# Performance work log

Measured on AMD Instinct MI355X. Metric: run time of the kernel, lower is better.

## Reference

```python
import jax, jax.numpy as jnp
import numpy as np


def _level_layout(depth, arity):
    counts = [arity ** (depth - 1 - l) for l in range(depth)]  # leaves first
    offs = np.concatenate([[0], np.cumsum(counts)]).astype(np.int64)
    return counts, offs


def _tree_lstm_forward(x, e2h_w, ioux_w, ioux_b, iouh_w, iouh_b,
                       fx_w, fx_b, fh_w, fh_b,
                       children_idx, edge_type, depth, arity):
    N = x.shape[0]
    H = fh_w.shape[0]
    E = e2h_w.shape[0]
    counts, offs = _level_layout(depth, arity)

    # state tables; row N is the zero-state sentinel for padded/leaf children
    h_all = jnp.zeros((N + 1, H), x.dtype)
    c_all = jnp.zeros((N + 1, H), x.dtype)

    # --- leaves (level 0): child_h_sum = 0, sum(f*child_c) = 0 ---
    nL = counts[0]
    iou = x[:nL] @ ioux_w.T + ioux_b + iouh_b  # iouh(0) = bias
    i, o, u = jnp.split(iou, 3, axis=1)
    c = jax.nn.sigmoid(i) * jnp.tanh(u)
    h = jax.nn.sigmoid(o) * jnp.tanh(c)
    c_all = c_all.at[:nL].set(c)
    h_all = h_all.at[:nL].set(h)

    # --- internal levels, bottom-up ---
    for l in range(1, depth):
        s, e = int(offs[l]), int(offs[l + 1])
        idx = children_idx[s:e]          # [M, C]
        et = edge_type[s:e]              # [M, C]
        ch_h = h_all[idx]                # [M, C, H]
        ch_c = c_all[idx]                # [M, C, H]
        xm = x[s:e]                      # [M, D]
        # edge-typed aggregation: sum_k W_{e_k} h_k = sum_e W_e (sum_{k: e_k=e} h_k)
        onehot = jax.nn.one_hot(et, E, dtype=x.dtype)       # [M, C, E]
        S = jnp.einsum('mce,mcj->mej', onehot, ch_h)        # [M, E, H]
        hsum = jnp.einsum('mej,eij->mi', S, e2h_w)          # [M, H]
        iou = xm @ ioux_w.T + ioux_b + hsum @ iouh_w.T + iouh_b
        i, o, u = jnp.split(iou, 3, axis=1)
        f = jax.nn.sigmoid(jnp.einsum('mcj,ij->mci', ch_h, fh_w) + fh_b
                           + (xm @ fx_w.T + fx_b)[:, None, :])  # [M, C, H]
        fc = (f * ch_c).sum(axis=1)                             # [M, H]
        c = jax.nn.sigmoid(i) * jnp.tanh(u) + fc
        h = jax.nn.sigmoid(o) * jnp.tanh(c)
        c_all = c_all.at[s:e].set(c)
        h_all = h_all.at[s:e].set(h)

    root = N - 1
    return c_all[root:root + 1], h_all[root:root + 1]


def setup_inputs() -> dict:
    key = jax.random.key(0)
    ks = jax.random.split(key, 12)
    depth, arity, E, H, D = 9, 4, 37, 256, 300
    counts, offs = _level_layout(depth, arity)
    N = int(offs[-1])  # 87381

    # complete arity-ary tree, reverse level order (leaves first, root last)
    children = np.full((N, arity), N, dtype=np.int32)  # sentinel N for leaves
    for l in range(1, depth):
        p = np.arange(counts[l])
        base = offs[l - 1] + p * arity
        children[offs[l]:offs[l + 1]] = (base[:, None] + np.arange(arity)[None, :]).astype(np.int32)

    sc = 0.05
    return {
        'x': jax.random.normal(ks[0], (N, D), jnp.float32),
        'children_idx': jnp.asarray(children),
        'edge_type': jax.random.randint(ks[1], (N, arity), 0, E, jnp.int32),
        'depth': depth,
        'arity': arity,
        'e2h_w': jax.random.normal(ks[2], (E, H, H), jnp.float32) * sc,
        'ioux_w': jax.random.normal(ks[3], (3 * H, D), jnp.float32) * sc,
        'ioux_b': jax.random.normal(ks[4], (3 * H,), jnp.float32) * sc,
        'iouh_w': jax.random.normal(ks[5], (3 * H, H), jnp.float32) * sc,
        'iouh_b': jax.random.normal(ks[6], (3 * H,), jnp.float32) * sc,
        'fx_w': jax.random.normal(ks[7], (H, D), jnp.float32) * sc,
        'fx_b': jax.random.normal(ks[8], (H,), jnp.float32) * sc,
        'fh_w': jax.random.normal(ks[9], (H, H), jnp.float32) * sc,
        'fh_b': jax.random.normal(ks[10], (H,), jnp.float32) * sc,
    }


def reference(x, children_idx, edge_type, depth, arity,
              e2h_w, ioux_w, ioux_b, iouh_w, iouh_b,
              fx_w, fx_b, fh_w, fh_b):
    return _tree_lstm_forward(x, e2h_w, ioux_w, ioux_b, iouh_w, iouh_b,
                              fx_w, fx_b, fh_w, fh_b,
                              children_idx, edge_type, depth, arity)
```

## Files before the change

### kernel.cpp

```cpp
#include <hip/hip_runtime.h>
#include <math.h>

#define H 256
#define D 300
#define NE 37
#define NLEAF 65536
#define NTOT 87381
#define NINT 21845
#define NICH 87380
#define PERMPAD 1184
#define KX 320
#define KN 576
#define NROWS 87424
#define NBINS 296
#define HB 120
#define CHUNK 729

typedef __attribute__((ext_vector_type(8))) short short8;
typedef __attribute__((ext_vector_type(4))) float f32x4;

__device__ const int g_offs[10] = {0,65536,81920,86016,87040,87296,87360,87376,87380,87381};
static const int h_offs[10]     = {0,65536,81920,86016,87040,87296,87360,87376,87380,87381};

__device__ __forceinline__ float frcp(float v){ return __builtin_amdgcn_rcpf(v); }
__device__ __forceinline__ float sigm(float v){ return frcp(1.0f + __expf(-v)); }
__device__ __forceinline__ float ftanh(float v){ return 1.0f - 2.0f*frcp(__expf(2.0f*v) + 1.0f); }
__device__ __forceinline__ unsigned short f2bf(float f){
  unsigned int u = __float_as_uint(f);
  return (unsigned short)((u + 0x7fffu + ((u>>16)&1u)) >> 16);
}
__device__ __forceinline__ float bf2f(unsigned short v){ return __uint_as_float(((unsigned int)v)<<16); }

__global__ void k_convx(const float* __restrict__ x, unsigned short* __restrict__ xb)
{
  size_t total = (size_t)NROWS*KX/8;
  for (size_t v8 = (size_t)blockIdx.x*blockDim.x + threadIdx.x; v8 < total;
       v8 += (size_t)gridDim.x*blockDim.x) {
    int p = (int)(v8/40), k0 = (int)(v8%40)*8;
    short8 o;
    #pragma unroll
    for (int j=0;j<8;j++){
      int k = k0+j;
      float v = (p < NTOT && k < D) ? x[(size_t)p*D + k] : 0.f;
      o[j] = (short)f2bf(v);
    }
    *reinterpret_cast<short8*>(xb + v8*8) = o;
  }
}

__global__ void k_convw(const float* __restrict__ ioux_w, const float* __restrict__ fx_w,
                        const float* __restrict__ iouh_w, const float* __restrict__ fh_w,
                        const float* __restrict__ e2h_w,
                        unsigned short* __restrict__ WN, unsigned short* __restrict__ WE)
{
  const int TOTN = 1024*KN;
  const int TOTE = NE*512*256;
  for (int idx = blockIdx.x*blockDim.x + threadIdx.x; idx < TOTN+TOTE;
       idx += gridDim.x*blockDim.x) {
    if (idx < TOTN) {
      int n = idx/KN, k = idx%KN;
      float v = 0.f;
      if (k < D)        v = (n < 768) ? ioux_w[n*D + k] : fx_w[(n-768)*D + k];
      else if (k >= KX && n < 768) v = iouh_w[n*H + (k-KX)];
      WN[idx] = f2bf(v);
    } else {
      int r = idx - TOTN;
      int e = r/(512*256), rr = r%(512*256), n = rr>>8, k = rr&255;
      float v = (n < 256) ? e2h_w[(size_t)e*65536 + n*256 + k] : fh_w[(n-256)*256 + k];
      WE[r] = f2bf(v);
    }
  }
}

__global__ void k_bias(const float* __restrict__ ioux_b, const float* __restrict__ iouh_b,
                       const float* __restrict__ fx_b, const float* __restrict__ fh_b,
                       float* __restrict__ bias)
{
  int n = blockIdx.x*blockDim.x + threadIdx.x;
  if (n < 768)       bias[n] = ioux_b[n] + iouh_b[n];
  else if (n < 1024) bias[n] = fx_b[n-768] + fh_b[n-768];
}

__device__ __forceinline__ int level_of(int g){
  int l = 1;
  #pragma unroll
  for (int q=2;q<=8;q++) if (g >= g_offs[q]) l = q;
  return l;
}

__global__ void k_hist2(const int* __restrict__ edge_type, int* __restrict__ bhist)
{
  __shared__ int hs[NBINS];
  int b = blockIdx.x, tid = threadIdx.x;
  for (int i = tid; i < NBINS; i += 256) hs[i] = 0;
  __syncthreads();
  int t0 = b*CHUNK, t1 = min(t0+CHUNK, NICH);
  for (int t = t0 + tid; t < t1; t += 256){
    int g = NLEAF + (t>>2);
    int l = level_of(g);
    int et = edge_type[g*4 + (t&3)];
    atomicAdd(&hs[(l-1)*NE + et], 1);
  }
  __syncthreads();
  for (int i = tid; i < NBINS; i += 256) bhist[b*NBINS + i] = hs[i];
}

__global__ void k_scan(const int* __restrict__ bhist, int* __restrict__ boff,
                       int* __restrict__ ptot)
{
  __shared__ int tot[NBINS];
  __shared__ int base[NBINS];
  int tid = threadIdx.x;
  if (tid < NBINS){
    int s = 0;
    for (int b=0;b<HB;b++) s += bhist[b*NBINS + tid];
    tot[tid] = s;
  }
  __syncthreads();
  if (tid < 8){
    int acc = 0;
    for (int e=0;e<NE;e++){
      base[tid*NE + e] = acc;
      acc += ((tot[tid*NE + e] + 31)>>5)<<5;
    }
    ptot[tid] = acc;
  }
  __syncthreads();
  if (tid < NBINS){
    int run = base[tid];
    for (int b=0;b<HB;b++){
      boff[b*NBINS + tid] = run;
      run += bhist[b*NBINS + tid];
    }
  }
}

__global__ void k_scatter2(const int* __restrict__ edge_type, const int* __restrict__ boff,
                           int* __restrict__ perm)
{
  __shared__ int cnt[NBINS];
  int b = blockIdx.x, tid = threadIdx.x;
  for (int i = tid; i < NBINS; i += 256) cnt[i] = boff[b*NBINS + i];
  __syncthreads();
  int t0 = b*CHUNK, t1 = min(t0+CHUNK, NICH);
  for (int t = t0 + tid; t < t1; t += 256){
    int g = NLEAF + (t>>2);
    int l = level_of(g);
    int c = t&3;
    int et = edge_type[g*4 + c];
    int p = g - g_offs[l];
    int pos = atomicAdd(&cnt[(l-1)*NE + et], 1);
    perm[g_offs[l-1] + (l-1)*PERMPAD + pos] = 4*p + c;
  }
}

template<int G>
__launch_bounds__(256, 2)
__global__ void k_gemm_gates(const unsigned short* __restrict__ A1, int lda1,
                             const unsigned short* __restrict__ A2, int lda2,
                             const unsigned short* __restrict__ WN,
                             const float* __restrict__ bias,
                             int M, int ksteps, int kc1,
                             const unsigned short* __restrict__ ybuf,
                             const float* __restrict__ c_child,
                             float* __restrict__ c_out,
                             unsigned short* __restrict__ h_out,
                             float* __restrict__ hroot, int rootrow)
{
  __shared__ __align__(16) unsigned short As[64*40];
  __shared__ __align__(16) unsigned short Bs[G*128*40];
  int m0 = blockIdx.x*64, n0r = blockIdx.y*128;
  int tid = threadIdx.x, lane = tid&63, wave = tid>>6;
  int wm = (wave&1)*32, wn = (wave>>1)*64;
  int ar = lane&15, kb = (lane>>4)*8;
  f32x4 acc[G][2][4] = {};

  for (int kc=0; kc<ksteps; ++kc){
    __syncthreads();
    {
      int row = tid>>2, seg = tid&3;
      int gm = m0 + row;
      short8 v = {0,0,0,0,0,0,0,0};
      if (gm < M){
        const unsigned short* p = (kc < kc1)
          ? (A1 + (size_t)gm*lda1 + kc*32 + seg*8)
          : (A2 + (size_t)gm*lda2 + (kc-kc1)*32 + seg*8);
        v = *reinterpret_cast<const short8*>(p);
      }
      *reinterpret_cast<short8*>(&As[row*40 + seg*8]) = v;
    }
    #pragma unroll
    for (int rep=0; rep<2*G; ++rep){
      int u = tid + rep*256;
      int row = u>>2, seg = u&3;
      int g = row>>7, rr2 = row&127;
      const unsigned short* q = WN + (size_t)(g*256 + n0r + rr2)*KN + kc*32 + seg*8;
      *reinterpret_cast<short8*>(&Bs[row*40 + seg*8]) = *reinterpret_cast<const short8*>(q);
    }
    __syncthreads();
    short8 af[2];
    #pragma unroll
    for (int mi=0; mi<2; ++mi)
      af[mi] = *reinterpret_cast<const short8*>(&As[(wm + mi*16 + ar)*40 + kb]);
    #pragma unroll
    for (int g=0; g<G; ++g){
      #pragma unroll
      for (int nj=0; nj<4; ++nj){
        short8 bfr = *reinterpret_cast<const short8*>(&Bs[(g*128 + wn + nj*16 + ar)*40 + kb]);
        #pragma unroll
        for (int mi=0; mi<2; ++mi)
          acc[g][mi][nj] = __builtin_amdgcn_mfma_f32_16x16x32_bf16(af[mi], bfr, acc[g][mi][nj], 0,0,0);
      }
    }
  }

  int rr = (lane>>4)*4, cc = lane&15;
  #pragma unroll
  for (int mi=0; mi<2; ++mi){
    #pragma unroll
    for (int r=0; r<4; ++r){
      int p = m0 + wm + mi*16 + rr + r;
      if (p < M){
        #pragma unroll
        for (int nj=0; nj<4; ++nj){
          int i = n0r + wn + nj*16 + cc;
          float ig = sigm (acc[0][mi][nj][r] + bias[i]);
          float og = sigm (acc[1][mi][nj][r] + bias[256+i]);
          float uu = ftanh(acc[2][mi][nj][r] + bias[512+i]);
          float ccv = ig*uu;
          if (G == 4){
            float fxv = acc[3][mi][nj][r] + bias[768+i];
            float fc = 0.f;
            #pragma unroll
            for (int c=0;c<4;c++){
              int k = 4*p + c;
              fc += sigm(bf2f(ybuf[(size_t)k*512 + 256 + i]) + fxv)
                    * c_child[(size_t)k*H + i];
            }
            ccv += fc;
          }
          float hh = og*ftanh(ccv);
          c_out[(size_t)p*H + i] = ccv;
          h_out[(size_t)p*H + i] = f2bf(hh);
          if (G == 4 && p == rootrow) hroot[i] = hh;
        }
      }
    }
  }
}

__launch_bounds__(256)
__global__ void k_gemm_ch(const unsigned short* __restrict__ hb, const int* __restrict__ edge_type,
                          const int* __restrict__ perm, const int* __restrict__ ptot,
                          const unsigned short* __restrict__ WE,
                          unsigned short* __restrict__ ybuf, int lvl)
{
  int childbase = g_offs[lvl-1];
  int nodebase  = g_offs[lvl];
  int permbase  = childbase + (lvl-1)*PERMPAD;
  int j0 = blockIdx.x*32;
  if (j0 >= ptot[lvl-1]) return;

  __shared__ __align__(16) unsigned short As[32*40];
  __shared__ __align__(16) unsigned short Bs[512*40];
  __shared__ int ks[32];
  int tid = threadIdx.x, lane = tid&63, wave = tid>>6;
  if (tid < 32) ks[tid] = perm[permbase + j0 + tid];
  __syncthreads();
  int k0 = ks[0];
  int e = edge_type[(nodebase + (k0>>2))*4 + (k0&3)];
  const unsigned short* WEe = WE + (size_t)e*512*256;
  f32x4 acc[2][8] = {};
  int ar = lane&15, kb = (lane>>4)*8;

  for (int kc=0; kc<8; ++kc){
    __syncthreads();
    if (tid < 128){
      int row = tid>>2, seg = tid&3;
      int k = ks[row];
      short8 v = {0,0,0,0,0,0,0,0};
      if (k >= 0)
        v = *reinterpret_cast<const short8*>(hb + (size_t)(childbase+k)*H + kc*32 + seg*8);
      *reinterpret_cast<short8*>(&As[row*40 + seg*8]) = v;
    }
    #pragma unroll
    for (int rep=0; rep<8; ++rep){
      int u = tid + rep*256;
      int row = u>>2, seg = u&3;
      *reinterpret_cast<short8*>(&Bs[row*40 + seg*8]) =
        *reinterpret_cast<const short8*>(WEe + (size_t)row*256 + kc*32 + seg*8);
    }
    __syncthreads();
    short8 af[2], bfr[8];
    af[0] = *reinterpret_cast<const short8*>(&As[(ar)*40 + kb]);
    af[1] = *reinterpret_cast<const short8*>(&As[(16+ar)*40 + kb]);
    #pragma unroll
    for (int j=0;j<8;j++)
      bfr[j] = *reinterpret_cast<const short8*>(&Bs[(wave*128 + j*16 + ar)*40 + kb]);
    #pragma unroll
    for (int i=0;i<2;i++)
      #pragma unroll
      for (int j=0;j<8;j++)
        acc[i][j] = __builtin_amdgcn_mfma_f32_16x16x32_bf16(af[i], bfr[j], acc[i][j], 0,0,0);
  }

  int rr = (lane>>4)*4, cc = lane&15;
  #pragma unroll
  for (int i=0;i<2;i++){
    #pragma unroll
    for (int r=0;r<4;r++){
      int ml = i*16 + rr + r;
      int k = ks[ml];
      if (k >= 0){
        #pragma unroll
        for (int j=0;j<8;j++){
          int n = wave*128 + j*16 + cc;
          ybuf[(size_t)k*512 + n] = f2bf(acc[i][j][r]);
        }
      }
    }
  }
}

__global__ void k_reduce4(const unsigned short* __restrict__ ybuf,
                          unsigned short* __restrict__ hsumb, int m)
{
  int u = blockIdx.x*blockDim.x + threadIdx.x;
  if (u >= m*32) return;
  int p = u>>5, i0 = (u&31)*8;
  float s[8] = {0,0,0,0,0,0,0,0};
  #pragma unroll
  for (int c=0;c<4;c++){
    short8 v = *reinterpret_cast<const short8*>(ybuf + (size_t)(4*p+c)*512 + i0);
    #pragma unroll
    for (int j=0;j<8;j++) s[j] += bf2f((unsigned short)v[j]);
  }
  short8 o;
  #pragma unroll
  for (int j=0;j<8;j++) o[j] = (short)f2bf(s[j]);
  *reinterpret_cast<short8*>(hsumb + (size_t)p*H + i0) = o;
}

__global__ void k_out(const float* __restrict__ c_all, const float* __restrict__ hroot,
                      float* __restrict__ out)
{
  int i = threadIdx.x;
  out[i]     = c_all[(size_t)(NTOT-1)*H + i];
  out[256+i] = hroot[i];
}

extern "C" void kernel_launch(void* const* d_in, const int* in_sizes, int n_in,
                              void* d_out, int out_size, void* d_ws, size_t ws_size,
                              hipStream_t stream)
{
  const float* x        = (const float*)d_in[0];
  const int*   edge_type= (const int*)d_in[2];
  const float* e2h_w    = (const float*)d_in[5];
  const float* ioux_w   = (const float*)d_in[6];
  const float* ioux_b   = (const float*)d_in[7];
  const float* iouh_w   = (const float*)d_in[8];
  const float* iouh_b   = (const float*)d_in[9];
  const float* fx_w     = (const float*)d_in[10];
  const float* fx_b     = (const float*)d_in[11];
  const float* fh_w     = (const float*)d_in[12];
  const float* fh_b     = (const float*)d_in[13];
  float* out = (float*)d_out;

  char* ws = (char*)d_ws;
  size_t o = 0;
  auto alloc = [&](size_t bytes){ size_t r = o; o += (bytes + 255) & ~(size_t)255; return r; };
  size_t off_xb    = alloc((size_t)NROWS*KX*2);
  size_t off_hb    = alloc((size_t)NROWS*H*2);
  size_t off_c     = alloc((size_t)NTOT*H*4);
  size_t off_WN    = alloc((size_t)1024*KN*2);
  size_t off_WE    = alloc((size_t)NE*512*256*2);
  size_t off_bias  = alloc(1024*4);
  size_t off_ybuf  = alloc((size_t)NLEAF*512*2);
  size_t off_hsumb = alloc((size_t)16384*H*2);
  size_t off_hroot = alloc(256*4);
  size_t off_perm  = alloc((size_t)(NICH + 8*PERMPAD)*4);
  size_t off_bhist = alloc((size_t)HB*NBINS*4);
  size_t off_boff  = alloc((size_t)HB*NBINS*4);
  size_t off_ptot  = alloc(8*4);

  unsigned short* xb    = (unsigned short*)(ws + off_xb);
  unsigned short* hb    = (unsigned short*)(ws + off_hb);
  float*          c_all = (float*)(ws + off_c);
  unsigned short* WN    = (unsigned short*)(ws + off_WN);
  unsigned short* WE    = (unsigned short*)(ws + off_WE);
  float*          bias  = (float*)(ws + off_bias);
  unsigned short* ybuf  = (unsigned short*)(ws + off_ybuf);
  unsigned short* hsumb = (unsigned short*)(ws + off_hsumb);
  float*          hroot = (float*)(ws + off_hroot);
  int* perm  = (int*)(ws + off_perm);
  int* bhist = (int*)(ws + off_bhist);
  int* boff  = (int*)(ws + off_boff);
  int* ptot  = (int*)(ws + off_ptot);

  hipMemsetAsync(perm, 0xFF, (size_t)(NICH + 8*PERMPAD)*4, stream);

  k_convx<<<2048, 256, 0, stream>>>(x, xb);
  k_convw<<<2048, 256, 0, stream>>>(ioux_w, fx_w, iouh_w, fh_w, e2h_w, WN, WE);
  k_bias <<<4, 256, 0, stream>>>(ioux_b, iouh_b, fx_b, fh_b, bias);
  k_hist2   <<<HB, 256, 0, stream>>>(edge_type, bhist);
  k_scan    <<<1, 512, 0, stream>>>(bhist, boff, ptot);
  k_scatter2<<<HB, 256, 0, stream>>>(edge_type, boff, perm);

  k_gemm_gates<3><<<dim3(NLEAF/64, 2), 256, 0, stream>>>(
      xb, KX, xb, KX, WN, bias, NLEAF, 10, 10,
      nullptr, nullptr, c_all, hb, nullptr, -1);

  for (int l=1; l<=8; ++l){
    int s    = h_offs[l];
    int m    = h_offs[l+1] - s;
    int childbase = h_offs[l-1];
    int nch  = s - childbase;
    int nblk = (nch + NE*31 + 31)/32;
    k_gemm_ch<<<nblk, 256, 0, stream>>>(hb, edge_type, perm, ptot, WE, ybuf, l);
    k_reduce4<<<(m*32+255)/256, 256, 0, stream>>>(ybuf, hsumb, m);
    k_gemm_gates<4><<<dim3((m+63)/64, 2), 256, 0, stream>>>(
        xb + (size_t)s*KX, KX, hsumb, H, WN, bias, m, 18, 10,
        ybuf, c_all + (size_t)childbase*H,
        c_all + (size_t)s*H, hb + (size_t)s*H,
        hroot, (l==8) ? 0 : -1);
  }
  k_out<<<1, 256, 0, stream>>>(c_all, hroot, out);
}
```

Measured before the change: 577.9 us.

## Fuse child-sum reduction into gates GEMM A-load, specialize leaf and internal kernels

Drops the separate k_reduce4 pass and its hsumb buffer. The internal-level gates kernel now sums the four children's projected h rows straight from ybuf while it loads the A tile. The templated gates kernel is split into a leaf kernel with no bounds checks and an internal kernel, and the launch bounds are raised so more blocks can be resident. This saves eight launches and one write and read of the hsum buffer per level. In exchange the A-tile load in every k-step reads four times as many bytes, and the higher occupancy targets may force register spills.

```diff
diff --git a/kernel.cpp b/kernel.cpp
--- a/kernel.cpp
+++ b/kernel.cpp
@@ -30,6 +30,7 @@
   return (unsigned short)((u + 0x7fffu + ((u>>16)&1u)) >> 16);
 }
 __device__ __forceinline__ float bf2f(unsigned short v){ return __uint_as_float(((unsigned int)v)<<16); }
+__device__ __forceinline__ short8 ld8(const unsigned short* p){ return *reinterpret_cast<const short8*>(p); }
 
 __global__ void k_convx(const float* __restrict__ x, unsigned short* __restrict__ xb)
 {
@@ -154,59 +155,203 @@
   }
 }
 
-template<int G>
-__launch_bounds__(256, 2)
-__global__ void k_gemm_gates(const unsigned short* __restrict__ A1, int lda1,
-                             const unsigned short* __restrict__ A2, int lda2,
+__launch_bounds__(256, 4)
+__global__ void k_leaf_gates(const unsigned short* __restrict__ xb,
                              const unsigned short* __restrict__ WN,
                              const float* __restrict__ bias,
-                             int M, int ksteps, int kc1,
-                             const unsigned short* __restrict__ ybuf,
-                             const float* __restrict__ c_child,
                              float* __restrict__ c_out,
-                             unsigned short* __restrict__ h_out,
-                             float* __restrict__ hroot, int rootrow)
+                             unsigned short* __restrict__ h_out)
 {
   __shared__ __align__(16) unsigned short As[64*40];
-  __shared__ __align__(16) unsigned short Bs[G*128*40];
+  __shared__ __align__(16) unsigned short Bs[3*128*40];
   int m0 = blockIdx.x*64, n0r = blockIdx.y*128;
   int tid = threadIdx.x, lane = tid&63, wave = tid>>6;
   int wm = (wave&1)*32, wn = (wave>>1)*64;
   int ar = lane&15, kb = (lane>>4)*8;
-  f32x4 acc[G][2][4] = {};
-
-  for (int kc=0; kc<ksteps; ++kc){
+  f32x4 acc[3][2][4] = {};
+
+  for (int kc=0; kc<10; ++kc){
+    __syncthreads();
+    {
+      int row = tid>>2, seg = tid&3;
+      *reinterpret_cast<short8*>(&As[row*40 + seg*8]) =
+        ld8(xb + (size_t)(m0+row)*KX + kc*32 + seg*8);
+    }
+    #pragma unroll
+    for (int rep=0; rep<6; ++rep){
+      int u = tid + rep*256;
+      int row = u>>2, seg = u&3;
+      int g = row>>7, rr2 = row&127;
+      *reinterpret_cast<short8*>(&Bs[row*40 + seg*8]) =
+        ld8(WN + (size_t)(g*256 + n0r + rr2)*KN + kc*32 + seg*8);
+    }
+    __syncthreads();
+    short8 af[2];
+    #pragma unroll
+    for (int mi=0; mi<2; ++mi)
+      af[mi] = ld8(&As[(wm + mi*16 + ar)*40 + kb]);
+    #pragma unroll
+    for (int g=0; g<3; ++g){
+      #pragma unroll
+      for (int nj=0; nj<4; ++nj){
+        short8 bfr = ld8(&Bs[(g*128 + wn + nj*16 + ar)*40 + kb]);
+        #pragma unroll
+        for (int mi=0; mi<2; ++mi)
+          acc[g][mi][nj] = __builtin_amdgcn_mfma_f32_16x16x32_bf16(af[mi], bfr, acc[g][mi][nj], 0,0,0);
+      }
+    }
+  }
+
+  int rr = (lane>>4)*4, cc = lane&15;
+  #pragma unroll
+  for (int mi=0; mi<2; ++mi){
+    #pragma unroll
+    for (int r=0; r<4; ++r){
+      int p = m0 + wm + mi*16 + rr + r;
+      #pragma unroll
+      for (int nj=0; nj<4; ++nj){
+        int i = n0r + wn + nj*16 + cc;
+        float ig = sigm (acc[0][mi][nj][r] + bias[i]);
+        float og = sigm (acc[1][mi][nj][r] + bias[256+i]);
+        float uu = ftanh(acc[2][mi][nj][r] + bias[512+i]);
+        float ccv = ig*uu;
+        float hh = og*ftanh(ccv);
+        c_out[(size_t)p*H + i] = ccv;
+        h_out[(size_t)p*H + i] = f2bf(hh);
+      }
+    }
+  }
+}
+
+__launch_bounds__(256, 3)
+__global__ void k_gemm_ch(const unsigned short* __restrict__ hb, const int* __restrict__ edge_type,
+                          const int* __restrict__ perm, const int* __restrict__ ptot,
+                          const unsigned short* __restrict__ WE,
+                          unsigned short* __restrict__ ybuf, int lvl)
+{
+  int childbase = g_offs[lvl-1];
+  int nodebase  = g_offs[lvl];
+  int permbase  = childbase + (lvl-1)*PERMPAD;
+  int j0 = blockIdx.x*32;
+  if (j0 >= ptot[lvl-1]) return;
+
+  __shared__ __align__(16) unsigned short As[32*40];
+  __shared__ __align__(16) unsigned short Bs[512*40];
+  __shared__ int ks[32];
+  int tid = threadIdx.x, lane = tid&63, wave = tid>>6;
+  if (tid < 32) ks[tid] = perm[permbase + j0 + tid];
+  __syncthreads();
+  int k0 = ks[0];
+  int e = edge_type[(nodebase + (k0>>2))*4 + (k0&3)];
+  const unsigned short* WEe = WE + (size_t)e*512*256;
+  f32x4 acc[2][8] = {};
+  int ar = lane&15, kb = (lane>>4)*8;
+
+  for (int kc=0; kc<8; ++kc){
+    __syncthreads();
+    if (tid < 128){
+      int row = tid>>2, seg = tid&3;
+      int k = ks[row];
+      short8 v = {0,0,0,0,0,0,0,0};
+      if (k >= 0)
+        v = ld8(hb + (size_t)(childbase+k)*H + kc*32 + seg*8);
+      *reinterpret_cast<short8*>(&As[row*40 + seg*8]) = v;
+    }
+    #pragma unroll
+    for (int rep=0; rep<8; ++rep){
+      int u = tid + rep*256;
+      int row = u>>2, seg = u&3;
+      *reinterpret_cast<short8*>(&Bs[row*40 + seg*8]) =
+        ld8(WEe + (size_t)row*256 + kc*32 + seg*8);
+    }
+    __syncthreads();
+    short8 af[2], bfr[8];
+    af[0] = ld8(&As[(ar)*40 + kb]);
+    af[1] = ld8(&As[(16+ar)*40 + kb]);
+    #pragma unroll
+    for (int j=0;j<8;j++)
+      bfr[j] = ld8(&Bs[(wave*128 + j*16 + ar)*40 + kb]);
+    #pragma unroll
+    for (int i=0;i<2;i++)
+      #pragma unroll
+      for (int j=0;j<8;j++)
+        acc[i][j] = __builtin_amdgcn_mfma_f32_16x16x32_bf16(af[i], bfr[j], acc[i][j], 0,0,0);
+  }
+
+  int rr = (lane>>4)*4, cc = lane&15;
+  #pragma unroll
+  for (int i=0;i<2;i++){
+    #pragma unroll
+    for (int r=0;r<4;r++){
+      int ml = i*16 + rr + r;
+      int k = ks[ml];
+      if (k >= 0){
+        #pragma unroll
+        for (int j=0;j<8;j++){
+          int n = wave*128 + j*16 + cc;
+          ybuf[(size_t)k*512 + n] = f2bf(acc[i][j][r]);
+        }
+      }
+    }
+  }
+}
+
+__launch_bounds__(256, 3)
+__global__ void k_gates4(const unsigned short* __restrict__ xb_lvl,
+                         const unsigned short* __restrict__ ybuf,
+                         const unsigned short* __restrict__ WN,
+                         const float* __restrict__ bias,
+                         const float* __restrict__ c_child,
+                         float* __restrict__ c_out,
+                         unsigned short* __restrict__ h_out,
+                         float* __restrict__ hroot, int rootrow, int M)
+{
+  __shared__ __align__(16) unsigned short As[64*40];
+  __shared__ __align__(16) unsigned short Bs[4*128*40];
+  int m0 = blockIdx.x*64, n0r = blockIdx.y*128;
+  int tid = threadIdx.x, lane = tid&63, wave = tid>>6;
+  int wm = (wave&1)*32, wn = (wave>>1)*64;
+  int ar = lane&15, kb = (lane>>4)*8;
+  f32x4 acc[4][2][4] = {};
+
+  for (int kc=0; kc<18; ++kc){
     __syncthreads();
     {
       int row = tid>>2, seg = tid&3;
       int gm = m0 + row;
       short8 v = {0,0,0,0,0,0,0,0};
       if (gm < M){
-        const unsigned short* p = (kc < kc1)
-          ? (A1 + (size_t)gm*lda1 + kc*32 + seg*8)
-          : (A2 + (size_t)gm*lda2 + (kc-kc1)*32 + seg*8);
-        v = *reinterpret_cast<const short8*>(p);
+        if (kc < 10){
+          v = ld8(xb_lvl + (size_t)gm*KX + kc*32 + seg*8);
+        } else {
+          const unsigned short* q = ybuf + (size_t)(4*gm)*512 + (kc-10)*32 + seg*8;
+          short8 a0 = ld8(q), a1 = ld8(q+512), a2 = ld8(q+1024), a3 = ld8(q+1536);
+          #pragma unroll
+          for (int j=0;j<8;j++)
+            v[j] = (short)f2bf(bf2f((unsigned short)a0[j]) + bf2f((unsigned short)a1[j])
+                             + bf2f((unsigned short)a2[j]) + bf2f((unsigned short)a3[j]));
+        }
       }
       *reinterpret_cast<short8*>(&As[row*40 + seg*8]) = v;
     }
     #pragma unroll
-    for (int rep=0; rep<2*G; ++rep){
+    for (int rep=0; rep<8; ++rep){
       int u = tid + rep*256;
       int row = u>>2, seg = u&3;
       int g = row>>7, rr2 = row&127;
-      const unsigned short* q = WN + (size_t)(g*256 + n0r + rr2)*KN + kc*32 + seg*8;
-      *reinterpret_cast<short8*>(&Bs[row*40 + seg*8]) = *reinterpret_cast<const short8*>(q);
+      *reinterpret_cast<short8*>(&Bs[row*40 + seg*8]) =
+        ld8(WN + (size_t)(g*256 + n0r + rr2)*KN + kc*32 + seg*8);
     }
     __syncthreads();
     short8 af[2];
     #pragma unroll
     for (int mi=0; mi<2; ++mi)
-      af[mi] = *reinterpret_cast<const short8*>(&As[(wm + mi*16 + ar)*40 + kb]);
-    #pragma unroll
-    for (int g=0; g<G; ++g){
+      af[mi] = ld8(&As[(wm + mi*16 + ar)*40 + kb]);
+    #pragma unroll
+    for (int g=0; g<4; ++g){
       #pragma unroll
       for (int nj=0; nj<4; ++nj){
-        short8 bfr = *reinterpret_cast<const short8*>(&Bs[(g*128 + wn + nj*16 + ar)*40 + kb]);
+        short8 bfr = ld8(&Bs[(g*128 + wn + nj*16 + ar)*40 + kb]);
         #pragma unroll
         for (int mi=0; mi<2; ++mi)
           acc[g][mi][nj] = __builtin_amdgcn_mfma_f32_16x16x32_bf16(af[mi], bfr, acc[g][mi][nj], 0,0,0);
@@ -227,118 +372,23 @@
           float ig = sigm (acc[0][mi][nj][r] + bias[i]);
           float og = sigm (acc[1][mi][nj][r] + bias[256+i]);
           float uu = ftanh(acc[2][mi][nj][r] + bias[512+i]);
-          float ccv = ig*uu;
-          if (G == 4){
-            float fxv = acc[3][mi][nj][r] + bias[768+i];
-            float fc = 0.f;
-            #pragma unroll
-            for (int c=0;c<4;c++){
-              int k = 4*p + c;
-              fc += sigm(bf2f(ybuf[(size_t)k*512 + 256 + i]) + fxv)
-                    * c_child[(size_t)k*H + i];
-            }
-            ccv += fc;
+          float fxv = acc[3][mi][nj][r] + bias[768+i];
+          float fc = 0.f;
+          #pragma unroll
+          for (int c=0;c<4;c++){
+            int k = 4*p + c;
+            fc += sigm(bf2f(ybuf[(size_t)k*512 + 256 + i]) + fxv)
+                  * c_child[(size_t)k*H + i];
           }
+          float ccv = ig*uu + fc;
           float hh = og*ftanh(ccv);
           c_out[(size_t)p*H + i] = ccv;
           h_out[(size_t)p*H + i] = f2bf(hh);
-          if (G == 4 && p == rootrow) hroot[i] = hh;
+          if (p == rootrow) hroot[i] = hh;
         }
       }
     }
   }
-}
-
-__launch_bounds__(256)
-__global__ void k_gemm_ch(const unsigned short* __restrict__ hb, const int* __restrict__ edge_type,
-                          const int* __restrict__ perm, const int* __restrict__ ptot,
-                          const unsigned short* __restrict__ WE,
-                          unsigned short* __restrict__ ybuf, int lvl)
-{
-  int childbase = g_offs[lvl-1];
-  int nodebase  = g_offs[lvl];
-  int permbase  = childbase + (lvl-1)*PERMPAD;
-  int j0 = blockIdx.x*32;
-  if (j0 >= ptot[lvl-1]) return;
-
-  __shared__ __align__(16) unsigned short As[32*40];
-  __shared__ __align__(16) unsigned short Bs[512*40];
-  __shared__ int ks[32];
-  int tid = threadIdx.x, lane = tid&63, wave = tid>>6;
-  if (tid < 32) ks[tid] = perm[permbase + j0 + tid];
-  __syncthreads();
-  int k0 = ks[0];
-  int e = edge_type[(nodebase + (k0>>2))*4 + (k0&3)];
-  const unsigned short* WEe = WE + (size_t)e*512*256;
-  f32x4 acc[2][8] = {};
-  int ar = lane&15, kb = (lane>>4)*8;
-
-  for (int kc=0; kc<8; ++kc){
-    __syncthreads();
-    if (tid < 128){
-      int row = tid>>2, seg = tid&3;
-      int k = ks[row];
-      short8 v = {0,0,0,0,0,0,0,0};
-      if (k >= 0)
-        v = *reinterpret_cast<const short8*>(hb + (size_t)(childbase+k)*H + kc*32 + seg*8);
-      *reinterpret_cast<short8*>(&As[row*40 + seg*8]) = v;
-    }
-    #pragma unroll
-    for (int rep=0; rep<8; ++rep){
-      int u = tid + rep*256;
-      int row = u>>2, seg = u&3;
-      *reinterpret_cast<short8*>(&Bs[row*40 + seg*8]) =
-        *reinterpret_cast<const short8*>(WEe + (size_t)row*256 + kc*32 + seg*8);
-    }
-    __syncthreads();
-    short8 af[2], bfr[8];
-    af[0] = *reinterpret_cast<const short8*>(&As[(ar)*40 + kb]);
-    af[1] = *reinterpret_cast<const short8*>(&As[(16+ar)*40 + kb]);
-    #pragma unroll
-    for (int j=0;j<8;j++)
-      bfr[j] = *reinterpret_cast<const short8*>(&Bs[(wave*128 + j*16 + ar)*40 + kb]);
-    #pragma unroll
-    for (int i=0;i<2;i++)
-      #pragma unroll
-      for (int j=0;j<8;j++)
-        acc[i][j] = __builtin_amdgcn_mfma_f32_16x16x32_bf16(af[i], bfr[j], acc[i][j], 0,0,0);
-  }
-
-  int rr = (lane>>4)*4, cc = lane&15;
-  #pragma unroll
-  for (int i=0;i<2;i++){
-    #pragma unroll
-    for (int r=0;r<4;r++){
-      int ml = i*16 + rr + r;
-      int k = ks[ml];
-      if (k >= 0){
-        #pragma unroll
-        for (int j=0;j<8;j++){
-          int n = wave*128 + j*16 + cc;
-          ybuf[(size_t)k*512 + n] = f2bf(acc[i][j][r]);
-        }
-      }
-    }
-  }
-}
-
-__global__ void k_reduce4(const unsigned short* __restrict__ ybuf,
-                          unsigned short* __restrict__ hsumb, int m)
-{
-  int u = blockIdx.x*blockDim.x + threadIdx.x;
-  if (u >= m*32) return;
-  int p = u>>5, i0 = (u&31)*8;
-  float s[8] = {0,0,0,0,0,0,0,0};
-  #pragma unroll
-  for (int c=0;c<4;c++){
-    short8 v = *reinterpret_cast<const short8*>(ybuf + (size_t)(4*p+c)*512 + i0);
-    #pragma unroll
-    for (int j=0;j<8;j++) s[j] += bf2f((unsigned short)v[j]);
-  }
-  short8 o;
-  #pragma unroll
-  for (int j=0;j<8;j++) o[j] = (short)f2bf(s[j]);
-  *reinterpret_cast<short8*>(hsumb + (size_t)p*H + i0) = o;
 }
 
 __global__ void k_out(const float* __restrict__ c_all, const float* __restrict__ hroot,
@@ -376,7 +426,6 @@
   size_t off_WE    = alloc((size_t)NE*512*256*2);
   size_t off_bias  = alloc(1024*4);
   size_t off_ybuf  = alloc((size_t)NLEAF*512*2);
-  size_t off_hsumb = alloc((size_t)16384*H*2);
   size_t off_hroot = alloc(256*4);
   size_t off_perm  = alloc((size_t)(NICH + 8*PERMPAD)*4);
   size_t off_bhist = alloc((size_t)HB*NBINS*4);
@@ -390,7 +439,6 @@
   unsigned short* WE    = (unsigned short*)(ws + off_WE);
   float*          bias  = (float*)(ws + off_bias);
   unsigned short* ybuf  = (unsigned short*)(ws + off_ybuf);
-  unsigned short* hsumb = (unsigned short*)(ws + off_hsumb);
   float*          hroot = (float*)(ws + off_hroot);
   int* perm  = (int*)(ws + off_perm);
   int* bhist = (int*)(ws + off_bhist);
@@ -406,9 +454,7 @@
   k_scan    <<<1, 512, 0, stream>>>(bhist, boff, ptot);
   k_scatter2<<<HB, 256, 0, stream>>>(edge_type, boff, perm);
 
-  k_gemm_gates<3><<<dim3(NLEAF/64, 2), 256, 0, stream>>>(
-      xb, KX, xb, KX, WN, bias, NLEAF, 10, 10,
-      nullptr, nullptr, c_all, hb, nullptr, -1);
+  k_leaf_gates<<<dim3(NLEAF/64, 2), 256, 0, stream>>>(xb, WN, bias, c_all, hb);
 
   for (int l=1; l<=8; ++l){
     int s    = h_offs[l];
@@ -417,12 +463,11 @@
     int nch  = s - childbase;
     int nblk = (nch + NE*31 + 31)/32;
     k_gemm_ch<<<nblk, 256, 0, stream>>>(hb, edge_type, perm, ptot, WE, ybuf, l);
-    k_reduce4<<<(m*32+255)/256, 256, 0, stream>>>(ybuf, hsumb, m);
-    k_gemm_gates<4><<<dim3((m+63)/64, 2), 256, 0, stream>>>(
-        xb + (size_t)s*KX, KX, hsumb, H, WN, bias, m, 18, 10,
-        ybuf, c_all + (size_t)childbase*H,
+    k_gates4<<<dim3((m+63)/64, 2), 256, 0, stream>>>(
+        xb + (size_t)s*KX, ybuf, WN, bias,
+        c_all + (size_t)childbase*H,
         c_all + (size_t)s*H, hb + (size_t)s*H,
-        hroot, (l==8) ? 0 : -1);
+        hroot, (l==8) ? 0 : -1, m);
   }
   k_out<<<1, 256, 0, stream>>>(c_all, hroot, out);
 }
```

New measurement: 904.5 us. +56.5%, slower.
